# Performance work log

Hardware: AMD Instinct MI355X
Metric: run time of the kernel (lower is better)

The kernel has to match this reference:

```python
import jax, jax.numpy as jnp
import numpy as np

N_ITERS = 100   # fixed ADMM (OSQP-style) iteration count
RHO = 1.0       # ADMM penalty
SIGMA = 1e-6    # OSQP regularization


def setup_inputs() -> dict:
    key = jax.random.key(0)
    ks = jax.random.split(key, 12)
    B, S, H, nA = 16384, 512, 1024, 24
    mEq, mIneq = 4, 8
    state = jax.random.normal(ks[0], (B, S), dtype=jnp.float32)
    Aeq = jax.random.normal(ks[1], (mEq, nA), dtype=jnp.float32)
    beq = jax.random.normal(ks[2], (mEq,), dtype=jnp.float32)
    A = jax.random.normal(ks[3], (mIneq, nA), dtype=jnp.float32)
    b = jax.random.uniform(ks[4], (mIneq,), dtype=jnp.float32)
    ub = jnp.ones((nA,), dtype=jnp.float32)
    lb = jnp.zeros((nA,), dtype=jnp.float32)
    # MLP parameters (3 Dense layers as in the flax module)
    W1 = jax.random.normal(ks[5], (S, H), dtype=jnp.float32) / np.sqrt(S).astype(np.float32)
    b1 = jnp.zeros((H,), dtype=jnp.float32)
    W2 = jax.random.normal(ks[6], (H, H), dtype=jnp.float32) / np.sqrt(H).astype(np.float32)
    b2 = jnp.zeros((H,), dtype=jnp.float32)
    W3 = jax.random.normal(ks[7], (H, nA), dtype=jnp.float32) / np.sqrt(H).astype(np.float32)
    b3 = jnp.zeros((nA,), dtype=jnp.float32)
    return dict(state=state, Aeq=Aeq, beq=beq, A=A, b=b, ub=ub, lb=lb,
                W1=W1, b1=b1, W2=W2, b2=b2, W3=W3, b3=b3)


def reference(state, Aeq, beq, A, b, ub, lb, W1, b1, W2, b2, W3, b3):
    # ---- 3-layer MLP ----
    h = jax.nn.relu(state @ W1 + b1)
    h = jax.nn.relu(h @ W2 + b2)
    raw = h @ W3 + b3                      # [B, n]
    n = raw.shape[-1]
    I = jnp.eye(n, dtype=raw.dtype)
    # ---- stack constraints exactly as solve_qp: [Aeq; A_ineq; I; -I] ----
    A_tot = jnp.concatenate([Aeq, A, I, -I], axis=0)            # [M, n]
    neg_inf = jnp.full((A.shape[0],), -jnp.inf, dtype=raw.dtype)
    l_tot = jnp.concatenate([beq, neg_inf, lb, -ub])            # [M]
    u_tot = jnp.concatenate([beq, b, ub, -lb])                  # [M]
    # ---- OSQP-style ADMM: min 0.5||x||^2 - raw'x  s.t. l <= A_tot x <= u ----
    q = -raw                                                    # [B, n]
    M = (1.0 + SIGMA) * I + RHO * (A_tot.T @ A_tot)             # [n, n] (P = I)
    Minv = jnp.linalg.inv(M)
    B_, m = q.shape[0], A_tot.shape[0]
    X0 = jnp.zeros_like(q)
    Z0 = jnp.zeros((B_, m), dtype=q.dtype)
    Y0 = jnp.zeros((B_, m), dtype=q.dtype)

    def step(carry, _):
        X, Z, Y = carry
        rhs = SIGMA * X - q + (RHO * Z - Y) @ A_tot             # [B, n]
        Xn = rhs @ Minv.T                                       # [B, n]
        Zt = Xn @ A_tot.T                                       # [B, m]
        Zn = jnp.clip(Zt + Y / RHO, l_tot, u_tot)
        Yn = Y + RHO * (Zt - Zn)
        return (Xn, Zn, Yn), None

    (X, Z, Y), _ = jax.lax.scan(step, (X0, Z0, Y0), None, length=N_ITERS)
    return X
```

## Files before the change

kernel.cpp:

```cpp
#include <hip/hip_runtime.h>

using uint = unsigned int;
using ushort = unsigned short;

typedef __attribute__((ext_vector_type(8))) short bf16x8;
typedef __attribute__((ext_vector_type(4))) short bf16x4;
typedef __attribute__((ext_vector_type(4))) float f32x4;

#define ADMM_ITERS 100
#define RHO_C 1.0f
#define SIGMA_C 1e-6f

__device__ inline ushort f2bf(float f) {
  union { float f; uint u; } c; c.f = f;
  uint u = c.u;
  uint r = (u + 0x7fffu + ((u >> 16) & 1u)) >> 16;
  return (ushort)r;
}

__device__ inline void gload_lds16(const void* g, void* l) {
  __builtin_amdgcn_global_load_lds(
      (const __attribute__((address_space(1))) void*)g,
      (__attribute__((address_space(3))) void*)l, 16, 0, 0);
}

__device__ inline void splitPack(const float* x, bf16x8& hi, bf16x8& lo) {
#pragma unroll
  for (int j = 0; j < 8; ++j) {
    uint b = __float_as_uint(x[j]);
    uint hb = b & 0xffff0000u;
    float lf = x[j] - __uint_as_float(hb);
    hi[j] = (short)(b >> 16);
    lo[j] = (short)(__float_as_uint(lf) >> 16);
  }
}

__device__ inline void packPairs(const f32x4& x, uint& h0, uint& h1,
                                 uint& l0, uint& l1) {
  uint b0 = __float_as_uint(x[0]), b1 = __float_as_uint(x[1]);
  uint b2 = __float_as_uint(x[2]), b3 = __float_as_uint(x[3]);
  float r0 = x[0] - __uint_as_float(b0 & 0xffff0000u);
  float r1 = x[1] - __uint_as_float(b1 & 0xffff0000u);
  float r2 = x[2] - __uint_as_float(b2 & 0xffff0000u);
  float r3 = x[3] - __uint_as_float(b3 & 0xffff0000u);
  h0 = __builtin_amdgcn_perm(b1, b0, 0x07060302u);
  h1 = __builtin_amdgcn_perm(b3, b2, 0x07060302u);
  l0 = __builtin_amdgcn_perm(__float_as_uint(r1), __float_as_uint(r0), 0x07060302u);
  l1 = __builtin_amdgcn_perm(__float_as_uint(r3), __float_as_uint(r2), 0x07060302u);
}

__device__ void transpose_body(const float* __restrict__ in, ushort* __restrict__ out,
                               int R, int C, int Cout, int bx, int by, int tid) {
  __shared__ float t[32][33];
  const int c0 = bx * 32, r0 = by * 32;
  const int tx = tid & 31, ty = tid >> 5;
  for (int rr = ty; rr < 32; rr += 8) {
    int r = r0 + rr, c = c0 + tx;
    float v = 0.0f;
    if (r < R && c < C) v = in[(long)r * C + c];
    t[rr][tx] = v;
  }
  __syncthreads();
  for (int rr = ty; rr < 32; rr += 8) {
    int c = c0 + rr, r = r0 + tx;
    if (c < Cout && r < R) out[(long)c * R + r] = f2bf(t[tx][rr]);
  }
}

__device__ void setup_body(const float* __restrict__ Aeq, const float* __restrict__ beq,
                           const float* __restrict__ A, const float* __restrict__ b,
                           const float* __restrict__ ub, const float* __restrict__ lb,
                           ushort* __restrict__ Th, ushort* __restrict__ Tl,
                           ushort* __restrict__ T0h, ushort* __restrict__ T0l,
                           float* __restrict__ blp, float* __restrict__ bup, int t) {
  __shared__ float Aug[24][48];
  __shared__ float A12[12 * 24];
  __shared__ float fac[24];
  __shared__ float Tx[24][36];
  for (int i = t; i < 48 * 64; i += 256) { Th[i] = 0; Tl[i] = 0; }
  for (int i = t; i < 48 * 32; i += 256) { T0h[i] = 0; T0l[i] = 0; }
  if (t < 96)  A12[t] = Aeq[t];
  if (t < 192) A12[96 + t] = A[t];
  __syncthreads();
  for (int idx = t; idx < 576; idx += 256) {
    int j = idx / 24, k = idx % 24;
    float s = (j == k) ? (1.0f + SIGMA_C + 2.0f * RHO_C) : 0.0f;
    for (int r = 0; r < 12; ++r) s += RHO_C * A12[r * 24 + j] * A12[r * 24 + k];
    Aug[j][k] = s;
    Aug[j][24 + k] = (j == k) ? 1.0f : 0.0f;
  }
  __syncthreads();
  for (int p = 0; p < 24; ++p) {
    float rp = 1.0f / Aug[p][p];
    if (t < 24) fac[t] = Aug[t][p];
    __syncthreads();
    if (t < 48) Aug[p][t] *= rp;
    __syncthreads();
    for (int idx = t; idx < 24 * 48; idx += 256) {
      int r = idx / 48, c = idx % 48;
      if (r != p) Aug[r][c] -= fac[r] * Aug[p][c];
    }
    __syncthreads();
  }
  auto splitStore = [](ushort* hp, ushort* lp, int i, float v) {
    ushort hs = f2bf(v);
    float hf = __uint_as_float(((uint)hs) << 16);
    ushort ls = f2bf(v - hf);
    hp[i] = hs; lp[i] = ls;
  };
  for (int idx = t; idx < 24 * 36; idx += 256) {
    int n = idx / 36, k = idx % 36;
    float v;
    if (k < 24) v = 2.0f * Aug[n][24 + k];
    else {
      v = 0.0f;
      for (int j = 0; j < 24; ++j) v += Aug[n][24 + j] * A12[(k - 24) * 24 + j];
    }
    Tx[n][k] = v;
    splitStore(Th, Tl, n * 64 + k, v);
  }
  __syncthreads();
  for (int idx = t; idx < 12 * 36; idx += 256) {
    int m = idx / 36, k = idx % 36;
    float v = 0.0f;
    for (int j = 0; j < 24; ++j) v += A12[m * 24 + j] * Tx[j][k];
    splitStore(Th, Tl, (24 + m) * 64 + k, v);
  }
  for (int idx = t; idx < 36 * 24; idx += 256) {
    int n = idx / 24, k = idx % 24;
    float v;
    if (n < 24) v = Aug[n][24 + k];
    else {
      v = 0.0f;
      for (int j = 0; j < 24; ++j) v += A12[(n - 24) * 24 + j] * Aug[j][24 + k];
    }
    splitStore(T0h, T0l, n * 32 + k, v);
  }
  if (t < 48) {
    float lv, uv;
    if (t < 24)      { lv = lb[t]; uv = ub[t]; }
    else if (t < 28) { lv = beq[t - 24]; uv = lv; }
    else if (t < 36) { lv = -1e30f; uv = b[t - 28]; }
    else             { lv = -1e30f; uv = 1e30f; }
    blp[t] = lv; bup[t] = uv;
  }
}

__global__ void prep_all(
    const float* __restrict__ state, ushort* __restrict__ stateB, int n4,
    const float* __restrict__ W1, ushort* __restrict__ W1T,
    const float* __restrict__ W2, ushort* __restrict__ W2T,
    const float* __restrict__ W3, ushort* __restrict__ W3T,
    const float* __restrict__ Aeq, const float* __restrict__ beq,
    const float* __restrict__ A, const float* __restrict__ b,
    const float* __restrict__ ub, const float* __restrict__ lb,
    ushort* __restrict__ Th, ushort* __restrict__ Tl,
    ushort* __restrict__ T0h, ushort* __restrict__ T0l,
    float* __restrict__ blp, float* __restrict__ bup) {
  const int nConv = n4 >> 8;
  int bb = blockIdx.x;
  if (bb < nConv) {
    int i = bb * 256 + threadIdx.x;
    if (i < n4) {
      float4 v = ((const float4*)state)[i];
      uint2 p;
      p.x = (uint)f2bf(v.x) | ((uint)f2bf(v.y) << 16);
      p.y = (uint)f2bf(v.z) | ((uint)f2bf(v.w) << 16);
      ((uint2*)stateB)[i] = p;
    }
    return;
  }
  bb -= nConv;
  if (bb < 512)  { transpose_body(W1, W1T, 512, 1024, 1024, bb & 31, bb >> 5, threadIdx.x); return; }
  bb -= 512;
  if (bb < 1024) { transpose_body(W2, W2T, 1024, 1024, 1024, bb & 31, bb >> 5, threadIdx.x); return; }
  bb -= 1024;
  if (bb < 32)   { transpose_body(W3, W3T, 1024, 24, 32, 0, bb, threadIdx.x); return; }
  setup_body(Aeq, beq, A, b, ub, lb, Th, Tl, T0h, T0l, blp, bup, threadIdx.x);
}

template<int BM, int BN, int WM, int WN, int TM, int TN, int MODE>
__global__ __launch_bounds__(256) void gemm_bt(
    const ushort* __restrict__ A, const ushort* __restrict__ Bt,
    const float* __restrict__ bias, void* __restrict__ Cout_,
    int K, int ldc, int nvalid) {
  __shared__ char lds[(BM + BN) * 64];
  char* ldsA = lds;
  char* ldsB = lds + BM * 64;

  const int tid = threadIdx.x;
  const int wave = tid >> 6;
  const int lane = tid & 63;
  const int blockM = blockIdx.y * BM;
  const int blockN = blockIdx.x * BN;
  const int wm = (wave / WN) * (TM * 16);
  const int wn = (wave % WN) * (TN * 16);

  f32x4 acc[TM][TN] = {};

  const int l15 = lane & 15;
  const int kq = lane >> 4;
  constexpr int AI = BM / 16;
  constexpr int TOT = (BM + BN) / 16;
  const int srow = lane >> 2;
  const int kb = (lane & 3) ^ ((srow >> 1) & 3);

  for (int k0 = 0; k0 < K; k0 += 32) {
    for (int inst = wave; inst < TOT; inst += 4) {
      const bool isA = inst < AI;
      const int i = isA ? inst : inst - AI;
      const ushort* gp = (isA ? A : Bt)
          + (long)((isA ? blockM : blockN) + i * 16 + srow) * K + (k0 + kb * 8);
      char* lp = (isA ? ldsA : ldsB) + i * 1024;
      gload_lds16(gp, lp);
    }
    __syncthreads();

    bf16x8 af[TM], bfr[TN];
#pragma unroll
    for (int i = 0; i < TM; ++i) {
      int r = wm + i * 16 + l15;
      int ch = kq ^ ((r >> 1) & 3);
      af[i] = *(const bf16x8*)(ldsA + r * 64 + ch * 16);
    }
#pragma unroll
    for (int j = 0; j < TN; ++j) {
      int r = wn + j * 16 + l15;
      int ch = kq ^ ((r >> 1) & 3);
      bfr[j] = *(const bf16x8*)(ldsB + r * 64 + ch * 16);
    }
#pragma unroll
    for (int i = 0; i < TM; ++i)
#pragma unroll
      for (int j = 0; j < TN; ++j)
        acc[i][j] = __builtin_amdgcn_mfma_f32_16x16x32_bf16(af[i], bfr[j], acc[i][j], 0, 0, 0);
    __syncthreads();
  }

  const int ro = lane >> 4;
#pragma unroll
  for (int i = 0; i < TM; ++i) {
#pragma unroll
    for (int j = 0; j < TN; ++j) {
      const int col = blockN + wn + j * 16 + l15;
      float bv;
      if (MODE == 0) bv = bias[col];
      else bv = (col < nvalid) ? bias[col] : 0.0f;
#pragma unroll
      for (int r = 0; r < 4; ++r) {
        const int row = blockM + wm + i * 16 + ro * 4 + r;
        float v = acc[i][j][r] + bv;
        if (MODE == 0) {
          v = fmaxf(v, 0.0f);
          ((ushort*)Cout_)[(long)row * ldc + col] = f2bf(v);
        } else {
          if (col < nvalid) ((float*)Cout_)[(long)row * ldc + col] = v;
        }
      }
    }
  }
}

#define GEMM8P_QUAD(MI0, NJ0)                                                 \
  _Pragma("unroll") for (int mi_ = 0; mi_ < 4; ++mi_)                         \
  _Pragma("unroll") for (int nj_ = 0; nj_ < 2; ++nj_)                         \
  _Pragma("unroll") for (int kk_ = 0; kk_ < 2; ++kk_)                         \
    acc[(MI0) + mi_][(NJ0) + nj_] = __builtin_amdgcn_mfma_f32_16x16x32_bf16(  \
        aF[mi_][kk_], bF[(NJ0) + nj_][kk_], acc[(MI0) + mi_][(NJ0) + nj_],    \
        0, 0, 0);

#define GEMM8P_SYNC_PRE()                              \
  __builtin_amdgcn_s_barrier();                        \
  asm volatile("s_waitcnt lgkmcnt(0)" ::: "memory");   \
  __builtin_amdgcn_sched_barrier(0);                   \
  __builtin_amdgcn_s_setprio(1);

#define GEMM8P_SYNC_POST()                             \
  __builtin_amdgcn_s_setprio(0);                       \
  __builtin_amdgcn_s_barrier();

__global__ __launch_bounds__(512, 2) void gemm8p(
    const ushort* __restrict__ A, const ushort* __restrict__ Bt,
    const float* __restrict__ bias, ushort* __restrict__ Cout,
    int K, int ldc, int nblk_n) {
  __shared__ __align__(16) char ldsc[131072];

  const int nwg = gridDim.x;
  const int bid = blockIdx.x;
  const int swz = (bid & 7) * (nwg >> 3) + (bid >> 3);
  const int blockM = (swz / nblk_n) * 256;
  const int blockN = (swz % nblk_n) * 256;

  const int tid = threadIdx.x;
  const int wave = tid >> 6;
  const int lane = tid & 63;
  const int l15 = lane & 15;
  const int q = lane >> 4;
  const int wm = (wave >> 2) * 128;
  const int wn = (wave & 3) * 64;
  const int nt = K >> 6;

  f32x4 acc[8][4] = {};

  auto stage = [&](int ts, int h) {
    if (ts >= nt) return;
    char* base = ldsc + ((ts & 1) << 16) + (h << 14);
#pragma unroll
    for (int j = 0; j < 2; ++j) {
      const int idx = wave * 64 + j * 512 + lane;
      const int row = idx >> 3;
      const int cs = (idx & 7) ^ (row & 7);
      const ushort* gp =
          (h < 2 ? A + (long)(blockM + ((h & 1) << 7) + row) * K
                 : Bt + (long)(blockN + ((h & 1) << 7) + row) * K)
          + (ts << 6) + cs * 8;
      gload_lds16(gp, base + ((wave * 64 + j * 512) << 4));
    }
  };
  auto dsA = [&](int cb, int mi, int kk) {
    const int r = wm + mi * 16 + l15;
    const int cs = (kk * 4 + q) ^ (r & 7);
    return *(const bf16x8*)(ldsc + (cb << 16) + r * 128 + cs * 16);
  };
  auto dsB = [&](int cb, int nj, int kk) {
    const int r = wn + nj * 16 + l15;
    const int cs = (kk * 4 + q) ^ (r & 7);
    return *(const bf16x8*)(ldsc + (cb << 16) + 32768 + r * 128 + cs * 16);
  };

  stage(0, 0); stage(0, 1); stage(0, 2); stage(0, 3);
  stage(1, 0);
  asm volatile("s_waitcnt vmcnt(2)" ::: "memory");
  __builtin_amdgcn_s_barrier();

  bf16x8 aF[4][2], bF[4][2];
#pragma unroll 1
  for (int t = 0; t < nt; ++t) {
    const int cb = t & 1;
#pragma unroll
    for (int mi = 0; mi < 4; ++mi)
#pragma unroll
      for (int kk = 0; kk < 2; ++kk) aF[mi][kk] = dsA(cb, mi, kk);
#pragma unroll
    for (int nj = 0; nj < 2; ++nj)
#pragma unroll
      for (int kk = 0; kk < 2; ++kk) bF[nj][kk] = dsB(cb, nj, kk);
    stage(t + 1, 1);
    GEMM8P_SYNC_PRE();
    GEMM8P_QUAD(0, 0);
    GEMM8P_SYNC_POST();
#pragma unroll
    for (int nj = 2; nj < 4; ++nj)
#pragma unroll
      for (int kk = 0; kk < 2; ++kk) bF[nj][kk] = dsB(cb, nj, kk);
    stage(t + 1, 2);
    GEMM8P_SYNC_PRE();
    GEMM8P_QUAD(0, 2);
    GEMM8P_SYNC_POST();
#pragma unroll
    for (int mi = 0; mi < 4; ++mi)
#pragma unroll
      for (int kk = 0; kk < 2; ++kk) aF[mi][kk] = dsA(cb, 4 + mi, kk);
    stage(t + 1, 3);
    GEMM8P_SYNC_PRE();
    GEMM8P_QUAD(4, 2);
    GEMM8P_SYNC_POST();
    stage(t + 2, 0);
    if (t + 2 < nt) { asm volatile("s_waitcnt vmcnt(2)" ::: "memory"); }
    else            { asm volatile("s_waitcnt vmcnt(0)" ::: "memory"); }
    __builtin_amdgcn_s_barrier();
    __builtin_amdgcn_s_setprio(1);
    GEMM8P_QUAD(4, 0);
    GEMM8P_SYNC_POST();
  }

#pragma unroll
  for (int mi = 0; mi < 8; ++mi) {
#pragma unroll
    for (int nj = 0; nj < 4; ++nj) {
      const int col = blockN + wn + nj * 16 + l15;
      const float bv = bias[col];
#pragma unroll
      for (int r = 0; r < 4; ++r) {
        const int row = blockM + wm + mi * 16 + q * 4 + r;
        float v = acc[mi][nj][r] + bv;
        v = fmaxf(v, 0.0f);
        Cout[(long)row * ldc + col] = f2bf(v);
      }
    }
  }
}

__global__ __launch_bounds__(256) void admm_mfma(
    const float* __restrict__ raw,
    const ushort* __restrict__ Th, const ushort* __restrict__ Tl,
    const ushort* __restrict__ T0h, const ushort* __restrict__ T0l,
    const float* __restrict__ blp, const float* __restrict__ bup,
    float* __restrict__ outp) {
  __shared__ __align__(16) float UL[4][1152];
  const int tid = threadIdx.x, wave = tid >> 6, lane = tid & 63;
  const int l15 = lane & 15, q = lane >> 4;
  const int bid = blockIdx.x;
  const bool dowrite = bid < 256;
  const long rowbase = (long)(bid & 255) * 64 + wave * 16;

  float* ubase = UL[wave];
  for (int i = lane; i < 1152; i += 64) ubase[i] = 0.0f;

  uint* uw = (uint*)ubase;
  uint* wpB = uw + 36 * l15 + 2 * q;
  const float* rpB = ubase + 36 * l15 + 4 * q;

  f32x4 bl[3], bu[3];
#pragma unroll
  for (int t = 0; t < 3; ++t) {
    bl[t] = *(const f32x4*)(blp + 16 * t + 4 * q);
    bu[t] = *(const f32x4*)(bup + 16 * t + 4 * q);
  }

  f32x4 W[3], base[3];
  {
    bf16x8 t0h[3], t0l[3];
#pragma unroll
    for (int t = 0; t < 3; ++t) {
      t0h[t] = *(const bf16x8*)(T0h + (16 * t + l15) * 32 + q * 8);
      t0l[t] = *(const bf16x8*)(T0l + (16 * t + l15) * 32 + q * 8);
    }
    float qa[8];
    if (q < 3) {
      const float* rp = raw + (rowbase + l15) * 24 + q * 8;
      float4 v0 = *(const float4*)rp;
      float4 v1 = *(const float4*)(rp + 4);
      qa[0] = v0.x; qa[1] = v0.y; qa[2] = v0.z; qa[3] = v0.w;
      qa[4] = v1.x; qa[5] = v1.y; qa[6] = v1.z; qa[7] = v1.w;
    } else {
#pragma unroll
      for (int j = 0; j < 8; ++j) qa[j] = 0.0f;
    }
    bf16x8 qhi, qlo;
    splitPack(qa, qhi, qlo);
#pragma unroll
    for (int t = 0; t < 3; ++t) {
      f32x4 acc = {0.0f, 0.0f, 0.0f, 0.0f};
      acc = __builtin_amdgcn_mfma_f32_16x16x32_bf16(t0h[t], qhi, acc, 0, 0, 0);
      acc = __builtin_amdgcn_mfma_f32_16x16x32_bf16(t0h[t], qlo, acc, 0, 0, 0);
      acc = __builtin_amdgcn_mfma_f32_16x16x32_bf16(t0l[t], qhi, acc, 0, 0, 0);
      base[t] = acc; W[t] = acc;
    }
  }

  bf16x8 th[3][2], tl[3][2];
#pragma unroll
  for (int t = 0; t < 3; ++t)
#pragma unroll
    for (int c = 0; c < 2; ++c) {
      th[t][c] = *(const bf16x8*)(Th + (16 * t + l15) * 64 + 32 * c + q * 8);
      tl[t][c] = *(const bf16x8*)(Tl + (16 * t + l15) * 64 + 32 * c + q * 8);
    }

#define PACKST(t, CC)                                                \
  {                                                                  \
    f32x4 u_;                                                        \
    _Pragma("unroll") for (int r = 0; r < 4; ++r) {                  \
      float w_ = W[t][r];                                            \
      float z_ = fminf(fmaxf(w_, bl[t][r]), bu[t][r]);               \
      float yy_ = w_ - z_;                                           \
      u_[r] = z_ - yy_;                                              \
      CC[r] = base[t][r] + yy_;                                      \
    }                                                                \
    uint h0_, h1_, l0_, l1_;                                         \
    packPairs(u_, h0_, h1_, l0_, l1_);                               \
    wpB[8 * t] = h0_; wpB[8 * t + 1] = h1_;                          \
    wpB[576 + 8 * t] = l0_; wpB[577 + 8 * t] = l1_;                  \
  }

#pragma unroll 1
  for (int it = 2; it < ADMM_ITERS; ++it) {
    f32x4 C0, C1, C2;
    PACKST(0, C0);
    PACKST(1, C1);
    PACKST(2, C2);
    bf16x8 uh0 = *(const bf16x8*)rpB;
    bf16x8 uh1 = *(const bf16x8*)(rpB + 16);
    bf16x8 ul0 = *(const bf16x8*)(rpB + 576);
    bf16x8 ul1 = *(const bf16x8*)(rpB + 592);
    f32x4 a0 = C0, a1 = C1, a2 = C2;
    a0 = __builtin_amdgcn_mfma_f32_16x16x32_bf16(th[0][0], uh0, a0, 0, 0, 0);
    a1 = __builtin_amdgcn_mfma_f32_16x16x32_bf16(th[1][0], uh0, a1, 0, 0, 0);
    a2 = __builtin_amdgcn_mfma_f32_16x16x32_bf16(th[2][0], uh0, a2, 0, 0, 0);
    a0 = __builtin_amdgcn_mfma_f32_16x16x32_bf16(th[0][1], uh1, a0, 0, 0, 0);
    a1 = __builtin_amdgcn_mfma_f32_16x16x32_bf16(th[1][1], uh1, a1, 0, 0, 0);
    a2 = __builtin_amdgcn_mfma_f32_16x16x32_bf16(th[2][1], uh1, a2, 0, 0, 0);
    a0 = __builtin_amdgcn_mfma_f32_16x16x32_bf16(th[0][0], ul0, a0, 0, 0, 0);
    a1 = __builtin_amdgcn_mfma_f32_16x16x32_bf16(th[1][0], ul0, a1, 0, 0, 0);
    a2 = __builtin_amdgcn_mfma_f32_16x16x32_bf16(th[2][0], ul0, a2, 0, 0, 0);
    a0 = __builtin_amdgcn_mfma_f32_16x16x32_bf16(th[0][1], ul1, a0, 0, 0, 0);
    a1 = __builtin_amdgcn_mfma_f32_16x16x32_bf16(th[1][1], ul1, a1, 0, 0, 0);
    a2 = __builtin_amdgcn_mfma_f32_16x16x32_bf16(th[2][1], ul1, a2, 0, 0, 0);
    a0 = __builtin_amdgcn_mfma_f32_16x16x32_bf16(tl[0][0], uh0, a0, 0, 0, 0);
    a1 = __builtin_amdgcn_mfma_f32_16x16x32_bf16(tl[1][0], uh0, a1, 0, 0, 0);
    a2 = __builtin_amdgcn_mfma_f32_16x16x32_bf16(tl[2][0], uh0, a2, 0, 0, 0);
    a0 = __builtin_amdgcn_mfma_f32_16x16x32_bf16(tl[0][1], uh1, a0, 0, 0, 0);
    a1 = __builtin_amdgcn_mfma_f32_16x16x32_bf16(tl[1][1], uh1, a1, 0, 0, 0);
    a2 = __builtin_amdgcn_mfma_f32_16x16x32_bf16(tl[2][1], uh1, a2, 0, 0, 0);
    W[0] = a0; W[1] = a1; W[2] = a2;
  }

  {
    f32x4 C0, C1, C2;
    PACKST(0, C0);
    PACKST(1, C1);
    PACKST(2, C2);
    bf16x8 uh0 = *(const bf16x8*)rpB;
    bf16x8 uh1 = *(const bf16x8*)(rpB + 16);
    bf16x8 ul0 = *(const bf16x8*)(rpB + 576);
    bf16x8 ul1 = *(const bf16x8*)(rpB + 592);
    f32x4 x0 = base[0], x1 = base[1];
    x0 = __builtin_amdgcn_mfma_f32_16x16x32_bf16(th[0][0], uh0, x0, 0, 0, 0);
    x1 = __builtin_amdgcn_mfma_f32_16x16x32_bf16(th[1][0], uh0, x1, 0, 0, 0);
    x0 = __builtin_amdgcn_mfma_f32_16x16x32_bf16(th[0][1], uh1, x0, 0, 0, 0);
    x1 = __builtin_amdgcn_mfma_f32_16x16x32_bf16(th[1][1], uh1, x1, 0, 0, 0);
    x0 = __builtin_amdgcn_mfma_f32_16x16x32_bf16(th[0][0], ul0, x0, 0, 0, 0);
    x1 = __builtin_amdgcn_mfma_f32_16x16x32_bf16(th[1][0], ul0, x1, 0, 0, 0);
    x0 = __builtin_amdgcn_mfma_f32_16x16x32_bf16(th[0][1], ul1, x0, 0, 0, 0);
    x1 = __builtin_amdgcn_mfma_f32_16x16x32_bf16(th[1][1], ul1, x1, 0, 0, 0);
    x0 = __builtin_amdgcn_mfma_f32_16x16x32_bf16(tl[0][0], uh0, x0, 0, 0, 0);
    x1 = __builtin_amdgcn_mfma_f32_16x16x32_bf16(tl[1][0], uh0, x1, 0, 0, 0);
    x0 = __builtin_amdgcn_mfma_f32_16x16x32_bf16(tl[0][1], uh1, x0, 0, 0, 0);
    x1 = __builtin_amdgcn_mfma_f32_16x16x32_bf16(tl[1][1], uh1, x1, 0, 0, 0);
    if (dowrite) {
      *(f32x4*)(outp + (rowbase + l15) * 24 + 4 * q) = x0;
      if (q < 2) *(f32x4*)(outp + (rowbase + l15) * 24 + 16 + 4 * q) = x1;
    }
  }
#undef PACKST
}

extern "C" void kernel_launch(void* const* d_in, const int* in_sizes, int n_in,
                              void* d_out, int out_size, void* d_ws, size_t ws_size,
                              hipStream_t stream) {
  const float* state = (const float*)d_in[0];
  const float* Aeq   = (const float*)d_in[1];
  const float* beq   = (const float*)d_in[2];
  const float* Ain   = (const float*)d_in[3];
  const float* bin   = (const float*)d_in[4];
  const float* ub    = (const float*)d_in[5];
  const float* lb    = (const float*)d_in[6];
  const float* W1    = (const float*)d_in[7];
  const float* b1    = (const float*)d_in[8];
  const float* W2    = (const float*)d_in[9];
  const float* b2    = (const float*)d_in[10];
  const float* W3    = (const float*)d_in[11];
  const float* b3    = (const float*)d_in[12];

  const int Bn = in_sizes[0] / 512;
  char* ws = (char*)d_ws;
  ushort* stateB = (ushort*)(ws + 0);
  ushort* W1T    = (ushort*)(ws + 16777216);
  ushort* W2T    = (ushort*)(ws + 17825792);
  ushort* W3T    = (ushort*)(ws + 19922944);
  ushort* Th     = (ushort*)(ws + 19993600);
  ushort* Tl     = (ushort*)(ws + 19999744);
  ushort* T0h    = (ushort*)(ws + 20005888);
  ushort* T0l    = (ushort*)(ws + 20008960);
  float*  blp    = (float*) (ws + 20012032);
  float*  bup    = (float*) (ws + 20012224);
  ushort* H1     = (ushort*)(ws + 21565440);
  ushort* H2     = (ushort*)(ws + 55119872);
  float*  rawb   = (float*)d_out;

  const int n4 = (Bn * 512) / 4;
  const int nConv = n4 / 256;
  const int nPrep = nConv + 512 + 1024 + 32 + 1;
  prep_all<<<nPrep, 256, 0, stream>>>(state, stateB, n4, W1, W1T, W2, W2T, W3, W3T,
                                      Aeq, beq, Ain, bin, ub, lb,
                                      Th, Tl, T0h, T0l, blp, bup);

  const int nblkN = 1024 / 256;
  const int nwg = (Bn / 256) * nblkN;
  gemm8p<<<nwg, 512, 0, stream>>>(stateB, W1T, b1, H1, 512, 1024, nblkN);
  gemm8p<<<nwg, 512, 0, stream>>>(H1, W2T, b2, H2, 1024, 1024, nblkN);
  gemm_bt<64, 32, 4, 1, 1, 2, 1><<<dim3(1, Bn / 64), 256, 0, stream>>>(
      H2, W3T, b3, rawb, 1024, 24, 24);

  admm_mfma<<<512, 256, 0, stream>>>(rawb, Th, Tl, T0h, T0l, blp, bup,
                                     (float*)d_out);
}
```

Measured before the change: 268.4 us.

## Permute ADMM operator rows so MFMA output feeds next iteration in registers

```diff
diff --git a/kernel.cpp b/kernel.cpp
--- a/kernel.cpp
+++ b/kernel.cpp
@@ -47,6 +47,14 @@
   h1 = __builtin_amdgcn_perm(b3, b2, 0x07060302u);
   l0 = __builtin_amdgcn_perm(__float_as_uint(r1), __float_as_uint(r0), 0x07060302u);
   l1 = __builtin_amdgcn_perm(__float_as_uint(r3), __float_as_uint(r2), 0x07060302u);
+}
+
+__device__ inline int permrow(int n) {
+  if (n < 32) {
+    int j = n & 7;
+    return ((j >> 2) << 4) + ((n >> 3) << 2) + (j & 3);
+  }
+  return n;
 }
 
 __device__ void transpose_body(const float* __restrict__ in, ushort* __restrict__ out,
@@ -117,14 +125,14 @@
       for (int j = 0; j < 24; ++j) v += Aug[n][24 + j] * A12[(k - 24) * 24 + j];
     }
     Tx[n][k] = v;
-    splitStore(Th, Tl, n * 64 + k, v);
+    splitStore(Th, Tl, permrow(n) * 64 + k, v);
   }
   __syncthreads();
   for (int idx = t; idx < 12 * 36; idx += 256) {
     int m = idx / 36, k = idx % 36;
     float v = 0.0f;
     for (int j = 0; j < 24; ++j) v += A12[m * 24 + j] * Tx[j][k];
-    splitStore(Th, Tl, (24 + m) * 64 + k, v);
+    splitStore(Th, Tl, permrow(24 + m) * 64 + k, v);
   }
   for (int idx = t; idx < 36 * 24; idx += 256) {
     int n = idx / 24, k = idx % 24;
@@ -134,7 +142,7 @@
       v = 0.0f;
       for (int j = 0; j < 24; ++j) v += A12[(n - 24) * 24 + j] * Aug[j][24 + k];
     }
-    splitStore(T0h, T0l, n * 32 + k, v);
+    splitStore(T0h, T0l, permrow(n) * 32 + k, v);
   }
   if (t < 48) {
     float lv, uv;
@@ -391,32 +399,23 @@
   }
 }
 
-__global__ __launch_bounds__(256) void admm_mfma(
+__global__ __launch_bounds__(64) void admm_mfma(
     const float* __restrict__ raw,
     const ushort* __restrict__ Th, const ushort* __restrict__ Tl,
     const ushort* __restrict__ T0h, const ushort* __restrict__ T0l,
     const float* __restrict__ blp, const float* __restrict__ bup,
     float* __restrict__ outp) {
-  __shared__ __align__(16) float UL[4][1152];
-  const int tid = threadIdx.x, wave = tid >> 6, lane = tid & 63;
+  const int lane = threadIdx.x & 63;
   const int l15 = lane & 15, q = lane >> 4;
-  const int bid = blockIdx.x;
-  const bool dowrite = bid < 256;
-  const long rowbase = (long)(bid & 255) * 64 + wave * 16;
-
-  float* ubase = UL[wave];
-  for (int i = lane; i < 1152; i += 64) ubase[i] = 0.0f;
-
-  uint* uw = (uint*)ubase;
-  uint* wpB = uw + 36 * l15 + 2 * q;
-  const float* rpB = ubase + 36 * l15 + 4 * q;
+  const long rowbase = (long)blockIdx.x * 16;
 
   f32x4 bl[3], bu[3];
-#pragma unroll
-  for (int t = 0; t < 3; ++t) {
-    bl[t] = *(const f32x4*)(blp + 16 * t + 4 * q);
-    bu[t] = *(const f32x4*)(bup + 16 * t + 4 * q);
-  }
+  bl[0] = *(const f32x4*)(blp + 8 * q);
+  bu[0] = *(const f32x4*)(bup + 8 * q);
+  bl[1] = *(const f32x4*)(blp + 8 * q + 4);
+  bu[1] = *(const f32x4*)(bup + 8 * q + 4);
+  bl[2] = *(const f32x4*)(blp + 32 + 4 * q);
+  bu[2] = *(const f32x4*)(bup + 32 + 4 * q);
 
   f32x4 W[3], base[3];
   {
@@ -458,82 +457,78 @@
       tl[t][c] = *(const bf16x8*)(Tl + (16 * t + l15) * 64 + 32 * c + q * 8);
     }
 
-#define PACKST(t, CC)                                                \
-  {                                                                  \
-    f32x4 u_;                                                        \
-    _Pragma("unroll") for (int r = 0; r < 4; ++r) {                  \
-      float w_ = W[t][r];                                            \
-      float z_ = fminf(fmaxf(w_, bl[t][r]), bu[t][r]);               \
-      float yy_ = w_ - z_;                                           \
-      u_[r] = z_ - yy_;                                              \
-      CC[r] = base[t][r] + yy_;                                      \
-    }                                                                \
-    uint h0_, h1_, l0_, l1_;                                         \
-    packPairs(u_, h0_, h1_, l0_, l1_);                               \
-    wpB[8 * t] = h0_; wpB[8 * t + 1] = h1_;                          \
-    wpB[576 + 8 * t] = l0_; wpB[577 + 8 * t] = l1_;                  \
+#define CLIPU(t, U_, CC)                                             \
+  _Pragma("unroll") for (int r = 0; r < 4; ++r) {                    \
+    float w_ = W[t][r];                                              \
+    float z_ = fminf(fmaxf(w_, bl[t][r]), bu[t][r]);                 \
+    float yy_ = w_ - z_;                                             \
+    U_[r] = z_ - yy_;                                                \
+    CC[r] = base[t][r] + yy_;                                        \
   }
 
 #pragma unroll 1
   for (int it = 2; it < ADMM_ITERS; ++it) {
-    f32x4 C0, C1, C2;
-    PACKST(0, C0);
-    PACKST(1, C1);
-    PACKST(2, C2);
-    bf16x8 uh0 = *(const bf16x8*)rpB;
-    bf16x8 uh1 = *(const bf16x8*)(rpB + 16);
-    bf16x8 ul0 = *(const bf16x8*)(rpB + 576);
-    bf16x8 ul1 = *(const bf16x8*)(rpB + 592);
+    f32x4 u0, u1, u2, C0, C1, C2;
+    CLIPU(0, u0, C0);
+    CLIPU(1, u1, C1);
+    CLIPU(2, u2, C2);
+    union { uint d[4]; bf16x8 v; } uh0, ul0, uh1, ul1;
+    packPairs(u0, uh0.d[0], uh0.d[1], ul0.d[0], ul0.d[1]);
+    packPairs(u1, uh0.d[2], uh0.d[3], ul0.d[2], ul0.d[3]);
+    packPairs(u2, uh1.d[0], uh1.d[1], ul1.d[0], ul1.d[1]);
+    uh1.d[2] = 0; uh1.d[3] = 0; ul1.d[2] = 0; ul1.d[3] = 0;
     f32x4 a0 = C0, a1 = C1, a2 = C2;
-    a0 = __builtin_amdgcn_mfma_f32_16x16x32_bf16(th[0][0], uh0, a0, 0, 0, 0);
-    a1 = __builtin_amdgcn_mfma_f32_16x16x32_bf16(th[1][0], uh0, a1, 0, 0, 0);
-    a2 = __builtin_amdgcn_mfma_f32_16x16x32_bf16(th[2][0], uh0, a2, 0, 0, 0);
-    a0 = __builtin_amdgcn_mfma_f32_16x16x32_bf16(th[0][1], uh1, a0, 0, 0, 0);
-    a1 = __builtin_amdgcn_mfma_f32_16x16x32_bf16(th[1][1], uh1, a1, 0, 0, 0);
-    a2 = __builtin_amdgcn_mfma_f32_16x16x32_bf16(th[2][1], uh1, a2, 0, 0, 0);
-    a0 = __builtin_amdgcn_mfma_f32_16x16x32_bf16(th[0][0], ul0, a0, 0, 0, 0);
-    a1 = __builtin_amdgcn_mfma_f32_16x16x32_bf16(th[1][0], ul0, a1, 0, 0, 0);
-    a2 = __builtin_amdgcn_mfma_f32_16x16x32_bf16(th[2][0], ul0, a2, 0, 0, 0);
-    a0 = __builtin_amdgcn_mfma_f32_16x16x32_bf16(th[0][1], ul1, a0, 0, 0, 0);
-    a1 = __builtin_amdgcn_mfma_f32_16x16x32_bf16(th[1][1], ul1, a1, 0, 0, 0);
-    a2 = __builtin_amdgcn_mfma_f32_16x16x32_bf16(th[2][1], ul1, a2, 0, 0, 0);
-    a0 = __builtin_amdgcn_mfma_f32_16x16x32_bf16(tl[0][0], uh0, a0, 0, 0, 0);
-    a1 = __builtin_amdgcn_mfma_f32_16x16x32_bf16(tl[1][0], uh0, a1, 0, 0, 0);
-    a2 = __builtin_amdgcn_mfma_f32_16x16x32_bf16(tl[2][0], uh0, a2, 0, 0, 0);
-    a0 = __builtin_amdgcn_mfma_f32_16x16x32_bf16(tl[0][1], uh1, a0, 0, 0, 0);
-    a1 = __builtin_amdgcn_mfma_f32_16x16x32_bf16(tl[1][1], uh1, a1, 0, 0, 0);
-    a2 = __builtin_amdgcn_mfma_f32_16x16x32_bf16(tl[2][1], uh1, a2, 0, 0, 0);
+    a0 = __builtin_amdgcn_mfma_f32_16x16x32_bf16(th[0][0], uh0.v, a0, 0, 0, 0);
+    a1 = __builtin_amdgcn_mfma_f32_16x16x32_bf16(th[1][0], uh0.v, a1, 0, 0, 0);
+    a2 = __builtin_amdgcn_mfma_f32_16x16x32_bf16(th[2][0], uh0.v, a2, 0, 0, 0);
+    a0 = __builtin_amdgcn_mfma_f32_16x16x32_bf16(th[0][1], uh1.v, a0, 0, 0, 0);
+    a1 = __builtin_amdgcn_mfma_f32_16x16x32_bf16(th[1][1], uh1.v, a1, 0, 0, 0);
+    a2 = __builtin_amdgcn_mfma_f32_16x16x32_bf16(th[2][1], uh1.v, a2, 0, 0, 0);
+    a0 = __builtin_amdgcn_mfma_f32_16x16x32_bf16(th[0][0], ul0.v, a0, 0, 0, 0);
+    a1 = __builtin_amdgcn_mfma_f32_16x16x32_bf16(th[1][0], ul0.v, a1, 0, 0, 0);
+    a2 = __builtin_amdgcn_mfma_f32_16x16x32_bf16(th[2][0], ul0.v, a2, 0, 0, 0);
+    a0 = __builtin_amdgcn_mfma_f32_16x16x32_bf16(th[0][1], ul1.v, a0, 0, 0, 0);
+    a1 = __builtin_amdgcn_mfma_f32_16x16x32_bf16(th[1][1], ul1.v, a1, 0, 0, 0);
+    a2 = __builtin_amdgcn_mfma_f32_16x16x32_bf16(th[2][1], ul1.v, a2, 0, 0, 0);
+    a0 = __builtin_amdgcn_mfma_f32_16x16x32_bf16(tl[0][0], uh0.v, a0, 0, 0, 0);
+    a1 = __builtin_amdgcn_mfma_f32_16x16x32_bf16(tl[1][0], uh0.v, a1, 0, 0, 0);
+    a2 = __builtin_amdgcn_mfma_f32_16x16x32_bf16(tl[2][0], uh0.v, a2, 0, 0, 0);
+    a0 = __builtin_amdgcn_mfma_f32_16x16x32_bf16(tl[0][1], uh1.v, a0, 0, 0, 0);
+    a1 = __builtin_amdgcn_mfma_f32_16x16x32_bf16(tl[1][1], uh1.v, a1, 0, 0, 0);
+    a2 = __builtin_amdgcn_mfma_f32_16x16x32_bf16(tl[2][1], uh1.v, a2, 0, 0, 0);
     W[0] = a0; W[1] = a1; W[2] = a2;
   }
 
   {
-    f32x4 C0, C1, C2;
-    PACKST(0, C0);
-    PACKST(1, C1);
-    PACKST(2, C2);
-    bf16x8 uh0 = *(const bf16x8*)rpB;
-    bf16x8 uh1 = *(const bf16x8*)(rpB + 16);
-    bf16x8 ul0 = *(const bf16x8*)(rpB + 576);
-    bf16x8 ul1 = *(const bf16x8*)(rpB + 592);
+    f32x4 u0, u1, u2, C0, C1, C2;
+    CLIPU(0, u0, C0);
+    CLIPU(1, u1, C1);
+    CLIPU(2, u2, C2);
+    union { uint d[4]; bf16x8 v; } uh0, ul0, uh1, ul1;
+    packPairs(u0, uh0.d[0], uh0.d[1], ul0.d[0], ul0.d[1]);
+    packPairs(u1, uh0.d[2], uh0.d[3], ul0.d[2], ul0.d[3]);
+    packPairs(u2, uh1.d[0], uh1.d[1], ul1.d[0], ul1.d[1]);
+    uh1.d[2] = 0; uh1.d[3] = 0; ul1.d[2] = 0; ul1.d[3] = 0;
     f32x4 x0 = base[0], x1 = base[1];
-    x0 = __builtin_amdgcn_mfma_f32_16x16x32_bf16(th[0][0], uh0, x0, 0, 0, 0);
-    x1 = __builtin_amdgcn_mfma_f32_16x16x32_bf16(th[1][0], uh0, x1, 0, 0, 0);
-    x0 = __builtin_amdgcn_mfma_f32_16x16x32_bf16(th[0][1], uh1, x0, 0, 0, 0);
-    x1 = __builtin_amdgcn_mfma_f32_16x16x32_bf16(th[1][1], uh1, x1, 0, 0, 0);
-    x0 = __builtin_amdgcn_mfma_f32_16x16x32_bf16(th[0][0], ul0, x0, 0, 0, 0);
-    x1 = __builtin_amdgcn_mfma_f32_16x16x32_bf16(th[1][0], ul0, x1, 0, 0, 0);
-    x0 = __builtin_amdgcn_mfma_f32_16x16x32_bf16(th[0][1], ul1, x0, 0, 0, 0);
-    x1 = __builtin_amdgcn_mfma_f32_16x16x32_bf16(th[1][1], ul1, x1, 0, 0, 0);
-    x0 = __builtin_amdgcn_mfma_f32_16x16x32_bf16(tl[0][0], uh0, x0, 0, 0, 0);
-    x1 = __builtin_amdgcn_mfma_f32_16x16x32_bf16(tl[1][0], uh0, x1, 0, 0, 0);
-    x0 = __builtin_amdgcn_mfma_f32_16x16x32_bf16(tl[0][1], uh1, x0, 0, 0, 0);
-    x1 = __builtin_amdgcn_mfma_f32_16x16x32_bf16(tl[1][1], uh1, x1, 0, 0, 0);
-    if (dowrite) {
-      *(f32x4*)(outp + (rowbase + l15) * 24 + 4 * q) = x0;
-      if (q < 2) *(f32x4*)(outp + (rowbase + l15) * 24 + 16 + 4 * q) = x1;
-    }
-  }
-#undef PACKST
+    x0 = __builtin_amdgcn_mfma_f32_16x16x32_bf16(th[0][0], uh0.v, x0, 0, 0, 0);
+    x1 = __builtin_amdgcn_mfma_f32_16x16x32_bf16(th[1][0], uh0.v, x1, 0, 0, 0);
+    x0 = __builtin_amdgcn_mfma_f32_16x16x32_bf16(th[0][1], uh1.v, x0, 0, 0, 0);
+    x1 = __builtin_amdgcn_mfma_f32_16x16x32_bf16(th[1][1], uh1.v, x1, 0, 0, 0);
+    x0 = __builtin_amdgcn_mfma_f32_16x16x32_bf16(th[0][0], ul0.v, x0, 0, 0, 0);
+    x1 = __builtin_amdgcn_mfma_f32_16x16x32_bf16(th[1][0], ul0.v, x1, 0, 0, 0);
+    x0 = __builtin_amdgcn_mfma_f32_16x16x32_bf16(th[0][1], ul1.v, x0, 0, 0, 0);
+    x1 = __builtin_amdgcn_mfma_f32_16x16x32_bf16(th[1][1], ul1.v, x1, 0, 0, 0);
+    x0 = __builtin_amdgcn_mfma_f32_16x16x32_bf16(tl[0][0], uh0.v, x0, 0, 0, 0);
+    x1 = __builtin_amdgcn_mfma_f32_16x16x32_bf16(tl[1][0], uh0.v, x1, 0, 0, 0);
+    x0 = __builtin_amdgcn_mfma_f32_16x16x32_bf16(tl[0][1], uh1.v, x0, 0, 0, 0);
+    x1 = __builtin_amdgcn_mfma_f32_16x16x32_bf16(tl[1][1], uh1.v, x1, 0, 0, 0);
+    if (q < 3) {
+      float* op = outp + (rowbase + l15) * 24 + 8 * q;
+      *(f32x4*)op = x0;
+      *(f32x4*)(op + 4) = x1;
+    }
+  }
+#undef CLIPU
 }
 
 extern "C" void kernel_launch(void* const* d_in, const int* in_sizes, int n_in,
@@ -583,6 +578,6 @@
   gemm_bt<64, 32, 4, 1, 1, 2, 1><<<dim3(1, Bn / 64), 256, 0, stream>>>(
       H2, W3T, b3, rawb, 1024, 24, 24);
 
-  admm_mfma<<<512, 256, 0, stream>>>(rawb, Th, Tl, T0h, T0l, blp, bup,
-                                     (float*)d_out);
-}
+  admm_mfma<<<Bn / 16, 64, 0, stream>>>(rawb, Th, Tl, T0h, T0l, blp, bup,
+                                        (float*)d_out);
+}
```

New measurement: 267.6 us. About the same (-0.3%).
